# Kernel tuning notes

Hardware: AMD Instinct MI355X
Metric: run time of the kernel (lower is better)

## Reference

```python
import jax, jax.numpy as jnp
import numpy as np

D_MODEL = 1024
D_HEAD = 64
M_BITS = 32


def setup_inputs() -> dict:
    key = jax.random.key(0)
    ks = jax.random.split(key, 6)
    B, N, M = 2, 2048, 2048
    Q = jax.random.normal(ks[0], (B, N, D_MODEL), dtype=jnp.float32)
    K = jax.random.normal(ks[1], (B, M, D_MODEL), dtype=jnp.float32)
    V = jax.random.normal(ks[2], (B, M, D_MODEL), dtype=jnp.float32)
    s = 1.0 / np.sqrt(D_MODEL)
    Wq = jax.random.normal(ks[3], (D_MODEL, M_BITS), dtype=jnp.float32) * s
    Wk = jax.random.normal(ks[4], (D_MODEL, M_BITS), dtype=jnp.float32) * s
    Wv = jax.random.normal(ks[5], (D_MODEL, D_HEAD), dtype=jnp.float32) * s
    temperature = jnp.ones((1,), dtype=jnp.float32)
    return {"Q": Q, "K": K, "V": V, "Wq": Wq, "Wk": Wk, "Wv": Wv,
            "temperature": temperature}


def tropical_matmul(A, Bt):
    # A: [B, N, m], Bt: [B, M, m] (already transposed form of [B, m, M])
    # (A \odot B)_{ij} = min_k (A_ik + B_kj)
    return jnp.min(A[:, :, None, :] + Bt[:, None, :, :], axis=-1)  # [B, N, M]


def reference(Q, K, V, Wq, Wk, Wv, temperature):
    # REWA tropical encoders (continuous): linear projections to m_bits
    Qt = jnp.einsum('bnd,dm->bnm', Q, Wq)   # [B, N, m_bits]
    Kt = jnp.einsum('bsd,dm->bsm', K, Wk)   # [B, M, m_bits]
    Vp = jnp.einsum('bsd,dh->bsh', V, Wv)   # [B, M, d_head]
    # tropical (min-plus) scores, negated so shorter paths score higher
    scores = -tropical_matmul(Qt, Kt)       # [B, N, M]
    scores = scores / jax.nn.softplus(temperature[0])
    attn = jax.nn.softmax(scores, axis=-1)  # [B, N, M]
    out = jnp.einsum('bnm,bmh->bnh', attn, Vp)  # [B, N, d_head]
    return out, attn
```

## Files before the change

kernel.cpp:

```cpp
#include <hip/hip_runtime.h>
#include <math.h>

#define DM 1024
#define NB 2048
#define MBITS 32
#define DH 64

typedef __attribute__((ext_vector_type(4))) float floatx4;
typedef __attribute__((ext_vector_type(8))) short shortx8;

__device__ __forceinline__ unsigned short f32_to_bf16(float f) {
    union { float f; unsigned u; } v; v.f = f;
    unsigned r = v.u + 0x7FFF + ((v.u >> 16) & 1);
    return (unsigned short)(r >> 16);
}

__device__ __forceinline__ void split2(float x0, float x1, unsigned& hp, unsigned& lp) {
    union { float f; unsigned u; } a, b; a.f = x0; b.f = x1;
    unsigned h0 = a.u & 0xFFFF0000u, h1 = b.u & 0xFFFF0000u;
    union { unsigned u; float f; } hf0, hf1; hf0.u = h0; hf1.u = h1;
    union { float f; unsigned u; } c, d;
    c.f = x0 - hf0.f;
    d.f = x1 - hf1.f;
    hp = (h0 >> 16) | h1;
    lp = (c.u >> 16) | (d.u & 0xFFFF0000u);
}

__global__ __launch_bounds__(256) void wprep_kernel(
    const float* __restrict__ Wq, const float* __restrict__ Wk,
    const float* __restrict__ Wv, unsigned short* __restrict__ Wf)
{
    int wv = blockIdx.x * 4 + (threadIdx.x >> 6);
    int l  = threadIdx.x & 63;
    const float* W; int C, kc32, ct;
    if (wv < 64)       { W = Wq; C = 32; kc32 = wv >> 1;  ct = wv & 1; }
    else if (wv < 128) { W = Wk; C = 32; int z = wv - 64;  kc32 = z >> 1; ct = z & 1; }
    else               { W = Wv; C = 64; int z = wv - 128; kc32 = z >> 2; ct = z & 3; }
    int k0 = kc32 * 32 + (l >> 4) * 8;
    int c  = ct * 16 + (l & 15);
    float x[8];
    #pragma unroll
    for (int j = 0; j < 8; ++j) x[j] = W[(size_t)(k0 + j) * C + c];
    unsigned hp[4], lp[4];
    #pragma unroll
    for (int j2 = 0; j2 < 4; ++j2) split2(x[2 * j2], x[2 * j2 + 1], hp[j2], lp[j2]);
    uint4 hv; hv.x = hp[0]; hv.y = hp[1]; hv.z = hp[2]; hv.w = hp[3];
    uint4 lv; lv.x = lp[0]; lv.y = lp[1]; lv.z = lp[2]; lv.w = lp[3];
    *(uint4*)&Wf[(size_t)wv * 1024 + l * 8]       = hv;
    *(uint4*)&Wf[(size_t)wv * 1024 + 512 + l * 8] = lv;
}

__global__ __launch_bounds__(256) void proj_mfma2_kernel(
    const float* __restrict__ Q, const float* __restrict__ K, const float* __restrict__ V,
    const unsigned short* __restrict__ Wf,
    float* __restrict__ Qt, float* __restrict__ Kt, unsigned short* __restrict__ VpT)
{
    __shared__ float red[4][64][16];

    int gb = blockIdx.x;
    int job = gb >> 8, tile = gb & 255;
    int r0 = tile * 16;
    const float* X = (job == 0) ? Q : (job == 1) ? K : V;
    int ntct  = (job == 2) ? 4 : 2;
    int pbase = job << 6;
    int t = threadIdx.x, w = t >> 6, l = t & 63;
    int lrow = l & 15, lq = l >> 4;

    const float* xrow = &X[(size_t)(r0 + lrow) * DM + w * 256 + lq * 8];

    floatx4 acc[4];
    #pragma unroll
    for (int i = 0; i < 4; ++i) acc[i] = (floatx4){0.f, 0.f, 0.f, 0.f};

    #pragma unroll
    for (int s = 0; s < 8; ++s) {
        floatx4 g0 = *(const floatx4*)(xrow + s * 32);
        floatx4 g1 = *(const floatx4*)(xrow + s * 32 + 4);
        union { unsigned u[4]; shortx8 v; } ahi, alo;
        split2(g0.x, g0.y, ahi.u[0], alo.u[0]);
        split2(g0.z, g0.w, ahi.u[1], alo.u[1]);
        split2(g1.x, g1.y, ahi.u[2], alo.u[2]);
        split2(g1.z, g1.w, ahi.u[3], alo.u[3]);
        int kc32 = w * 8 + s;
        #pragma unroll
        for (int ct = 0; ct < 4; ++ct) {
            if (ct >= ntct) break;
            int p = pbase + kc32 * ntct + ct;
            const unsigned short* wp = &Wf[(size_t)p * 1024 + l * 8];
            shortx8 bhi = *(const shortx8*)wp;
            shortx8 blo = *(const shortx8*)(wp + 512);
            acc[ct] = __builtin_amdgcn_mfma_f32_16x16x32_bf16(ahi.v, bhi, acc[ct], 0, 0, 0);
            acc[ct] = __builtin_amdgcn_mfma_f32_16x16x32_bf16(ahi.v, blo, acc[ct], 0, 0, 0);
            acc[ct] = __builtin_amdgcn_mfma_f32_16x16x32_bf16(alo.v, bhi, acc[ct], 0, 0, 0);
        }
    }

    #pragma unroll
    for (int ct = 0; ct < 4; ++ct) {
        if (ct >= ntct) break;
        #pragma unroll
        for (int r = 0; r < 4; ++r) red[w][l][ct * 4 + r] = acc[ct][r];
    }
    __syncthreads();

    int row = r0 + lq * 4 + w;
    if (job < 2) {
        float* Y = (job == 0) ? Qt : Kt;
        #pragma unroll
        for (int ct = 0; ct < 2; ++ct) {
            float v = red[0][l][ct * 4 + w] + red[1][l][ct * 4 + w]
                    + red[2][l][ct * 4 + w] + red[3][l][ct * 4 + w];
            Y[(size_t)row * MBITS + ct * 16 + lrow] = v;
        }
    } else {
        int b = row >> 11, j = row & 2047;
        #pragma unroll
        for (int ct = 0; ct < 4; ++ct) {
            float v = red[0][l][ct * 4 + w] + red[1][l][ct * 4 + w]
                    + red[2][l][ct * 4 + w] + red[3][l][ct * 4 + w];
            VpT[(size_t)b * (DH * NB) + (size_t)(ct * 16 + lrow) * NB + j] = f32_to_bf16(v);
        }
    }
}

template <typename ET>
__global__ __launch_bounds__(256) void trop_score_kernel(
    const float* __restrict__ Qt, const float* __restrict__ Kt,
    const float* __restrict__ temp, float* __restrict__ partial,
    ET* __restrict__ ebuf)
{
    __shared__ float Qs[16][36];
    __shared__ float Ks[256][36];

    int b  = blockIdx.z;
    int jc = blockIdx.y;
    int i0 = blockIdx.x * 16;
    int t  = threadIdx.x;
    int w  = t >> 6, l = t & 63;

    if (t < 128) {
        int row = t >> 3, k4 = t & 7;
        *(floatx4*)&Qs[row][k4 * 4] =
            *(const floatx4*)&Qt[(size_t)(b * NB + i0 + row) * MBITS + k4 * 4];
    }
    #pragma unroll
    for (int u = 0; u < 8; ++u) {
        int flat4 = u * 256 + t;
        int row = flat4 >> 3, k4 = flat4 & 7;
        *(floatx4*)&Ks[row][k4 * 4] =
            *(const floatx4*)&Kt[(size_t)(b * NB + jc * 256 + row) * MBITS + k4 * 4];
    }
    float tv = temp[0];
    float c2 = -(1.0f / log1pf(__expf(tv))) * 1.44269504088896340736f;
    __syncthreads();

    float m[4][4];
    #pragma unroll
    for (int ii = 0; ii < 4; ++ii)
        #pragma unroll
        for (int jj = 0; jj < 4; ++jj) m[ii][jj] = 1e30f;

    #pragma unroll
    for (int k4 = 0; k4 < 8; ++k4) {
        floatx4 q[4], kk[4];
        #pragma unroll
        for (int ii = 0; ii < 4; ++ii) q[ii] = *(const floatx4*)&Qs[w + 4 * ii][k4 * 4];
        #pragma unroll
        for (int jj = 0; jj < 4; ++jj) kk[jj] = *(const floatx4*)&Ks[l + 64 * jj][k4 * 4];
        #pragma unroll
        for (int ii = 0; ii < 4; ++ii)
            #pragma unroll
            for (int jj = 0; jj < 4; ++jj) {
                float a0 = q[ii].x + kk[jj].x;
                float a1 = q[ii].y + kk[jj].y;
                float a2 = q[ii].z + kk[jj].z;
                float a3 = q[ii].w + kk[jj].w;
                m[ii][jj] = fminf(fminf(m[ii][jj], fminf(a0, a1)), fminf(a2, a3));
            }
    }

    float psum[4];
    #pragma unroll
    for (int ii = 0; ii < 4; ++ii) {
        int i = w + 4 * ii;
        float s = 0.f;
        #pragma unroll
        for (int jj = 0; jj < 4; ++jj) {
            int j = l + 64 * jj;
            float e = exp2f(c2 * m[ii][jj]);
            size_t idx = (size_t)(b * NB + i0 + i) * 2048 + jc * 256 + j;
            if (sizeof(ET) == 2) ebuf[idx] = (ET)f32_to_bf16(e);
            else                 ebuf[idx] = (ET)e;
            s += e;
        }
        psum[ii] = s;
    }

    #pragma unroll
    for (int ii = 0; ii < 4; ++ii) {
        float v = psum[ii];
        #pragma unroll
        for (int off = 1; off < 64; off <<= 1) v += __shfl_xor(v, off, 64);
        if (l == 0) partial[((size_t)b * NB + i0 + w + 4 * ii) * 8 + jc] = v;
    }
}

template <bool EBF16>
__global__ __launch_bounds__(256) void trop_out_kernel(
    const unsigned short* __restrict__ VpT, const float* __restrict__ partial,
    const void* __restrict__ ebuf_in, float* __restrict__ outp, float* __restrict__ attn)
{
    __shared__ unsigned short Vs[64][256];
    __shared__ unsigned short Es[16][264];
    __shared__ float inv_s[16];

    int b  = blockIdx.z;
    int jc = blockIdx.y;
    int i0 = blockIdx.x * 16;
    int t  = threadIdx.x;
    int w  = t >> 6, l = t & 63;

    #pragma unroll
    for (int u = 0; u < 8; ++u) {
        int flat16 = u * 256 + t;
        int h = flat16 >> 5, c = flat16 & 31;
        uint4 g = *(const uint4*)&VpT[(size_t)b * (DH * NB) + (size_t)h * NB + jc * 256 + c * 8];
        *(uint4*)&Vs[h][(c ^ (h & 31)) * 8] = g;
    }
    if (t < 16) {
        float s = 0.f;
        #pragma unroll
        for (int p = 0; p < 8; ++p) s += partial[((size_t)b * NB + i0 + t) * 8 + p];
        inv_s[t] = 1.0f / s;
    }

    if (EBF16) {
        const unsigned short* eb = (const unsigned short*)ebuf_in;
        #pragma unroll
        for (int u = 0; u < 2; ++u) {
            int flat = u * 256 + t;
            int row = flat >> 5, c = flat & 31;
            uint4 g = *(const uint4*)&eb[(size_t)(b * NB + i0 + row) * 2048 + jc * 256 + c * 8];
            *(uint4*)&Es[row][c * 8] = g;
        }
        __syncthreads();
        int row = t >> 4, cb = (t & 15) * 16;
        float iv = inv_s[row];
        #pragma unroll
        for (int h8 = 0; h8 < 2; ++h8) {
            uint4 e8 = *(const uint4*)&Es[row][cb + h8 * 8];
            unsigned uu[4] = {e8.x, e8.y, e8.z, e8.w};
            float f[8];
            #pragma unroll
            for (int z = 0; z < 4; ++z) {
                union { unsigned u; float f; } v0, v1;
                v0.u = uu[z] << 16; v1.u = uu[z] & 0xFFFF0000u;
                f[2 * z] = v0.f * iv; f[2 * z + 1] = v1.f * iv;
            }
            size_t gidx = (size_t)(b * NB + i0 + row) * 2048 + jc * 256 + cb + h8 * 8;
            floatx4 o0; o0.x = f[0]; o0.y = f[1]; o0.z = f[2]; o0.w = f[3];
            floatx4 o1; o1.x = f[4]; o1.y = f[5]; o1.z = f[6]; o1.w = f[7];
            *(floatx4*)&attn[gidx]     = o0;
            *(floatx4*)&attn[gidx + 4] = o1;
        }
    } else {
        __syncthreads();
        #pragma unroll
        for (int u = 0; u < 4; ++u) {
            int flat4 = u * 256 + t;
            int row = flat4 >> 6, c4 = flat4 & 63;
            size_t g = (size_t)(b * NB + i0 + row) * 2048 + jc * 256 + c4 * 4;
            floatx4 e4 = *(const floatx4*)&attn[g];
            float iv = inv_s[row];
            unsigned u0 = (unsigned)f32_to_bf16(e4.x) | ((unsigned)f32_to_bf16(e4.y) << 16);
            unsigned u1 = (unsigned)f32_to_bf16(e4.z) | ((unsigned)f32_to_bf16(e4.w) << 16);
            uint2 pk; pk.x = u0; pk.y = u1;
            *(uint2*)&Es[row][c4 * 4] = pk;
            e4.x *= iv; e4.y *= iv; e4.z *= iv; e4.w *= iv;
            *(floatx4*)&attn[g] = e4;
        }
    }
    __syncthreads();

    floatx4 acc = {0.f, 0.f, 0.f, 0.f};
    #pragma unroll
    for (int kk = 0; kk < 8; ++kk) {
        int mrow = l & 15, q4 = l >> 4;
        shortx8 a = *(const shortx8*)&Es[mrow][kk * 32 + q4 * 8];
        int h = w * 16 + mrow;
        int c = kk * 4 + q4;
        shortx8 bf = *(const shortx8*)&Vs[h][(c ^ (h & 31)) * 8];
        acc = __builtin_amdgcn_mfma_f32_16x16x32_bf16(a, bf, acc, 0, 0, 0);
    }

    #pragma unroll
    for (int r = 0; r < 4; ++r) {
        int irow = (l >> 4) * 4 + r;
        atomicAdd(&outp[(size_t)(b * NB + i0 + irow) * DH + w * 16 + (l & 15)],
                  acc[r] * inv_s[irow]);
    }
}

extern "C" void kernel_launch(void* const* d_in, const int* in_sizes, int n_in,
                              void* d_out, int out_size, void* d_ws, size_t ws_size,
                              hipStream_t stream) {
    (void)in_sizes; (void)n_in; (void)out_size;
    const float* Q    = (const float*)d_in[0];
    const float* K    = (const float*)d_in[1];
    const float* V    = (const float*)d_in[2];
    const float* Wq   = (const float*)d_in[3];
    const float* Wk   = (const float*)d_in[4];
    const float* Wv   = (const float*)d_in[5];
    const float* temp = (const float*)d_in[6];

    float* outp = (float*)d_out;
    float* attn = outp + 2 * 2048 * 64;

    char* ws = (char*)d_ws;
    float*          Qt      = (float*)(ws);
    float*          Kt      = (float*)(ws + 524288);
    float*          partial = (float*)(ws + 1048576);
    unsigned short* Wf      = (unsigned short*)(ws + 1179648);
    unsigned short* VpT     = (unsigned short*)(ws + 1703936);
    unsigned short* Ebuf    = (unsigned short*)(ws + 2228224);
    bool bf16path = ws_size >= (size_t)2228224 + 16777216;

    hipMemsetAsync(d_out, 0, 262144 * sizeof(float), stream);

    wprep_kernel<<<64, 256, 0, stream>>>(Wq, Wk, Wv, Wf);
    proj_mfma2_kernel<<<768, 256, 0, stream>>>(Q, K, V, Wf, Qt, Kt, VpT);

    if (bf16path) {
        trop_score_kernel<unsigned short><<<dim3(128, 8, 2), 256, 0, stream>>>(
            Qt, Kt, temp, partial, Ebuf);
        trop_out_kernel<true><<<dim3(128, 8, 2), 256, 0, stream>>>(
            VpT, partial, Ebuf, outp, attn);
    } else {
        trop_score_kernel<float><<<dim3(128, 8, 2), 256, 0, stream>>>(
            Qt, Kt, temp, partial, attn);
        trop_out_kernel<false><<<dim3(128, 8, 2), 256, 0, stream>>>(
            VpT, partial, attn, outp, attn);
    }
}
```

Baseline: 151.4 us.

## Fuse tropical score and attention-output kernels into one full-row block kernel

Replaces the separate score kernel (which wrote bf16 exp values and per-chunk partial sums to global memory) and the output kernel with a single 1024-thread kernel. Each block computes a full 16x2048 score row in LDS, so it can reduce row sums locally, normalise, write attn and run the PV MFMA with double-buffered V tiles. This removes the intermediate E buffer round trip, the partial-sum buffer, the memset and the atomicAdds on the output. In exchange the grid shrinks to 256 large blocks with heavy LDS use, which lowers occupancy, and Q/K are now read directly from global memory instead of staged through LDS.

After: 344.5 us. +127.6%, slower.

```diff
diff --git a/kernel.cpp b/kernel.cpp
--- a/kernel.cpp
+++ b/kernel.cpp
@@ -123,188 +123,149 @@
     }
 }
 
-template <typename ET>
-__global__ __launch_bounds__(256) void trop_score_kernel(
+__global__ __launch_bounds__(1024) void fused_score_out_kernel(
     const float* __restrict__ Qt, const float* __restrict__ Kt,
-    const float* __restrict__ temp, float* __restrict__ partial,
-    ET* __restrict__ ebuf)
+    const unsigned short* __restrict__ VpT, const float* __restrict__ temp,
+    float* __restrict__ outp, float* __restrict__ attn)
 {
-    __shared__ float Qs[16][36];
-    __shared__ float Ks[256][36];
-
-    int b  = blockIdx.z;
-    int jc = blockIdx.y;
-    int i0 = blockIdx.x * 16;
-    int t  = threadIdx.x;
-    int w  = t >> 6, l = t & 63;
-
-    if (t < 128) {
-        int row = t >> 3, k4 = t & 7;
-        *(floatx4*)&Qs[row][k4 * 4] =
-            *(const floatx4*)&Qt[(size_t)(b * NB + i0 + row) * MBITS + k4 * 4];
-    }
-    #pragma unroll
-    for (int u = 0; u < 8; ++u) {
-        int flat4 = u * 256 + t;
-        int row = flat4 >> 3, k4 = flat4 & 7;
-        *(floatx4*)&Ks[row][k4 * 4] =
-            *(const floatx4*)&Kt[(size_t)(b * NB + jc * 256 + row) * MBITS + k4 * 4];
-    }
-    float tv = temp[0];
-    float c2 = -(1.0f / log1pf(__expf(tv))) * 1.44269504088896340736f;
-    __syncthreads();
-
-    float m[4][4];
-    #pragma unroll
-    for (int ii = 0; ii < 4; ++ii)
-        #pragma unroll
-        for (int jj = 0; jj < 4; ++jj) m[ii][jj] = 1e30f;
+    __shared__ unsigned short Elds[16][2056];
+    __shared__ unsigned short Vsb[2][64][256];
+    __shared__ float redsum[16][8];
+    __shared__ float inv_s[16];
+    __shared__ float redC[16][64][4];
+
+    const int b  = blockIdx.y;
+    const int i0 = blockIdx.x * 16;
+    const int t  = threadIdx.x;
+    const int w  = t >> 6, l = t & 63;
+    const int wr = w & 1;
+    const int wj = w >> 1;
+    const int jb = wj * 256 + l * 4;
+
+    const float tv = temp[0];
+    const float c2 = -(1.0f / log1pf(__expf(tv))) * 1.44269504088896340736f;
+
+    const float* Krow = &Kt[(size_t)(b * NB + jb) * MBITS];
+    const float* Qrow = &Qt[(size_t)(b * NB + i0 + wr * 8) * MBITS];
+
+    float m[8][4];
+    #pragma unroll
+    for (int r = 0; r < 8; ++r)
+        #pragma unroll
+        for (int jj = 0; jj < 4; ++jj) m[r][jj] = 1e30f;
 
     #pragma unroll
     for (int k4 = 0; k4 < 8; ++k4) {
-        floatx4 q[4], kk[4];
-        #pragma unroll
-        for (int ii = 0; ii < 4; ++ii) q[ii] = *(const floatx4*)&Qs[w + 4 * ii][k4 * 4];
-        #pragma unroll
-        for (int jj = 0; jj < 4; ++jj) kk[jj] = *(const floatx4*)&Ks[l + 64 * jj][k4 * 4];
-        #pragma unroll
-        for (int ii = 0; ii < 4; ++ii)
+        floatx4 kk[4];
+        #pragma unroll
+        for (int jj = 0; jj < 4; ++jj)
+            kk[jj] = *(const floatx4*)&Krow[jj * MBITS + k4 * 4];
+        #pragma unroll
+        for (int r = 0; r < 8; ++r) {
+            floatx4 q = *(const floatx4*)&Qrow[r * MBITS + k4 * 4];
             #pragma unroll
             for (int jj = 0; jj < 4; ++jj) {
-                float a0 = q[ii].x + kk[jj].x;
-                float a1 = q[ii].y + kk[jj].y;
-                float a2 = q[ii].z + kk[jj].z;
-                float a3 = q[ii].w + kk[jj].w;
-                m[ii][jj] = fminf(fminf(m[ii][jj], fminf(a0, a1)), fminf(a2, a3));
+                float a0 = q.x + kk[jj].x;
+                float a1 = q.y + kk[jj].y;
+                float a2 = q.z + kk[jj].z;
+                float a3 = q.w + kk[jj].w;
+                m[r][jj] = fminf(fminf(m[r][jj], fminf(a0, a1)), fminf(a2, a3));
             }
-    }
-
-    float psum[4];
-    #pragma unroll
-    for (int ii = 0; ii < 4; ++ii) {
-        int i = w + 4 * ii;
-        float s = 0.f;
-        #pragma unroll
-        for (int jj = 0; jj < 4; ++jj) {
-            int j = l + 64 * jj;
-            float e = exp2f(c2 * m[ii][jj]);
-            size_t idx = (size_t)(b * NB + i0 + i) * 2048 + jc * 256 + j;
-            if (sizeof(ET) == 2) ebuf[idx] = (ET)f32_to_bf16(e);
-            else                 ebuf[idx] = (ET)e;
-            s += e;
-        }
-        psum[ii] = s;
-    }
-
-    #pragma unroll
-    for (int ii = 0; ii < 4; ++ii) {
-        float v = psum[ii];
-        #pragma unroll
-        for (int off = 1; off < 64; off <<= 1) v += __shfl_xor(v, off, 64);
-        if (l == 0) partial[((size_t)b * NB + i0 + w + 4 * ii) * 8 + jc] = v;
-    }
-}
-
-template <bool EBF16>
-__global__ __launch_bounds__(256) void trop_out_kernel(
-    const unsigned short* __restrict__ VpT, const float* __restrict__ partial,
-    const void* __restrict__ ebuf_in, float* __restrict__ outp, float* __restrict__ attn)
-{
-    __shared__ unsigned short Vs[64][256];
-    __shared__ unsigned short Es[16][264];
-    __shared__ float inv_s[16];
-
-    int b  = blockIdx.z;
-    int jc = blockIdx.y;
-    int i0 = blockIdx.x * 16;
-    int t  = threadIdx.x;
-    int w  = t >> 6, l = t & 63;
-
-    #pragma unroll
-    for (int u = 0; u < 8; ++u) {
-        int flat16 = u * 256 + t;
-        int h = flat16 >> 5, c = flat16 & 31;
-        uint4 g = *(const uint4*)&VpT[(size_t)b * (DH * NB) + (size_t)h * NB + jc * 256 + c * 8];
-        *(uint4*)&Vs[h][(c ^ (h & 31)) * 8] = g;
-    }
+        }
+    }
+
+    #pragma unroll
+    for (int r = 0; r < 8; ++r) {
+        float e0 = exp2f(c2 * m[r][0]);
+        float e1 = exp2f(c2 * m[r][1]);
+        float e2 = exp2f(c2 * m[r][2]);
+        float e3 = exp2f(c2 * m[r][3]);
+        uint2 pk;
+        pk.x = (unsigned)f32_to_bf16(e0) | ((unsigned)f32_to_bf16(e1) << 16);
+        pk.y = (unsigned)f32_to_bf16(e2) | ((unsigned)f32_to_bf16(e3) << 16);
+        *(uint2*)&Elds[wr * 8 + r][jb] = pk;
+        float s = (e0 + e1) + (e2 + e3);
+        #pragma unroll
+        for (int off = 1; off < 64; off <<= 1) s += __shfl_xor(s, off, 64);
+        if (l == 0) redsum[w][r] = s;
+    }
+    __syncthreads();
+
     if (t < 16) {
         float s = 0.f;
         #pragma unroll
-        for (int p = 0; p < 8; ++p) s += partial[((size_t)b * NB + i0 + t) * 8 + p];
+        for (int g = 0; g < 8; ++g) s += redsum[(t >> 3) + 2 * g][t & 7];
         inv_s[t] = 1.0f / s;
     }
 
-    if (EBF16) {
-        const unsigned short* eb = (const unsigned short*)ebuf_in;
-        #pragma unroll
-        for (int u = 0; u < 2; ++u) {
-            int flat = u * 256 + t;
-            int row = flat >> 5, c = flat & 31;
-            uint4 g = *(const uint4*)&eb[(size_t)(b * NB + i0 + row) * 2048 + jc * 256 + c * 8];
-            *(uint4*)&Es[row][c * 8] = g;
+    const int sh = t >> 5, sc = t & 31;
+    {
+        uint4 g0 = *(const uint4*)&VpT[(size_t)b * (DH * NB) + (size_t)sh * NB + sc * 8];
+        uint4 g1 = *(const uint4*)&VpT[(size_t)b * (DH * NB) + (size_t)(sh + 32) * NB + sc * 8];
+        *(uint4*)&Vsb[0][sh][(sc ^ (sh & 31)) * 8]             = g0;
+        *(uint4*)&Vsb[0][sh + 32][(sc ^ ((sh + 32) & 31)) * 8] = g1;
+    }
+    __syncthreads();
+
+    const int mrow = l & 15, q4 = l >> 4;
+    const int hh  = (w & 3) * 16 + mrow;
+    const int kg  = w >> 2;
+    const int vsw = hh & 31;
+    const float iv = inv_s[w];
+    floatx4 acc = {0.f, 0.f, 0.f, 0.f};
+    int pb = 0;
+
+    for (int jc2 = 0; jc2 < 8; ++jc2) {
+        uint4 g0, g1;
+        if (jc2 < 7) {
+            g0 = *(const uint4*)&VpT[(size_t)b * (DH * NB) + (size_t)sh * NB + (jc2 + 1) * 256 + sc * 8];
+            g1 = *(const uint4*)&VpT[(size_t)b * (DH * NB) + (size_t)(sh + 32) * NB + (jc2 + 1) * 256 + sc * 8];
+        }
+        #pragma unroll
+        for (int t2 = 0; t2 < 2; ++t2) {
+            int ks = kg * 2 + t2;
+            shortx8 a = *(const shortx8*)&Elds[mrow][jc2 * 256 + ks * 32 + q4 * 8];
+            int c = ks * 4 + q4;
+            shortx8 bf = *(const shortx8*)&Vsb[pb][hh][(c ^ vsw) * 8];
+            acc = __builtin_amdgcn_mfma_f32_16x16x32_bf16(a, bf, acc, 0, 0, 0);
+        }
+        {
+            uint2 pk = *(const uint2*)&Elds[w][jc2 * 256 + l * 4];
+            union { unsigned u; float f; } x0, x1, x2, x3;
+            x0.u = pk.x << 16; x1.u = pk.x & 0xFFFF0000u;
+            x2.u = pk.y << 16; x3.u = pk.y & 0xFFFF0000u;
+            floatx4 o;
+            o.x = x0.f * iv; o.y = x1.f * iv; o.z = x2.f * iv; o.w = x3.f * iv;
+            *(floatx4*)&attn[(size_t)(b * NB + i0 + w) * 2048 + jc2 * 256 + l * 4] = o;
+        }
+        if (jc2 < 7) {
+            *(uint4*)&Vsb[pb ^ 1][sh][(sc ^ (sh & 31)) * 8]             = g0;
+            *(uint4*)&Vsb[pb ^ 1][sh + 32][(sc ^ ((sh + 32) & 31)) * 8] = g1;
         }
         __syncthreads();
-        int row = t >> 4, cb = (t & 15) * 16;
-        float iv = inv_s[row];
-        #pragma unroll
-        for (int h8 = 0; h8 < 2; ++h8) {
-            uint4 e8 = *(const uint4*)&Es[row][cb + h8 * 8];
-            unsigned uu[4] = {e8.x, e8.y, e8.z, e8.w};
-            float f[8];
-            #pragma unroll
-            for (int z = 0; z < 4; ++z) {
-                union { unsigned u; float f; } v0, v1;
-                v0.u = uu[z] << 16; v1.u = uu[z] & 0xFFFF0000u;
-                f[2 * z] = v0.f * iv; f[2 * z + 1] = v1.f * iv;
-            }
-            size_t gidx = (size_t)(b * NB + i0 + row) * 2048 + jc * 256 + cb + h8 * 8;
-            floatx4 o0; o0.x = f[0]; o0.y = f[1]; o0.z = f[2]; o0.w = f[3];
-            floatx4 o1; o1.x = f[4]; o1.y = f[5]; o1.z = f[6]; o1.w = f[7];
-            *(floatx4*)&attn[gidx]     = o0;
-            *(floatx4*)&attn[gidx + 4] = o1;
-        }
-    } else {
-        __syncthreads();
-        #pragma unroll
-        for (int u = 0; u < 4; ++u) {
-            int flat4 = u * 256 + t;
-            int row = flat4 >> 6, c4 = flat4 & 63;
-            size_t g = (size_t)(b * NB + i0 + row) * 2048 + jc * 256 + c4 * 4;
-            floatx4 e4 = *(const floatx4*)&attn[g];
-            float iv = inv_s[row];
-            unsigned u0 = (unsigned)f32_to_bf16(e4.x) | ((unsigned)f32_to_bf16(e4.y) << 16);
-            unsigned u1 = (unsigned)f32_to_bf16(e4.z) | ((unsigned)f32_to_bf16(e4.w) << 16);
-            uint2 pk; pk.x = u0; pk.y = u1;
-            *(uint2*)&Es[row][c4 * 4] = pk;
-            e4.x *= iv; e4.y *= iv; e4.z *= iv; e4.w *= iv;
-            *(floatx4*)&attn[g] = e4;
-        }
-    }
-    __syncthreads();
-
-    floatx4 acc = {0.f, 0.f, 0.f, 0.f};
-    #pragma unroll
-    for (int kk = 0; kk < 8; ++kk) {
-        int mrow = l & 15, q4 = l >> 4;
-        shortx8 a = *(const shortx8*)&Es[mrow][kk * 32 + q4 * 8];
-        int h = w * 16 + mrow;
-        int c = kk * 4 + q4;
-        shortx8 bf = *(const shortx8*)&Vs[h][(c ^ (h & 31)) * 8];
-        acc = __builtin_amdgcn_mfma_f32_16x16x32_bf16(a, bf, acc, 0, 0, 0);
-    }
-
-    #pragma unroll
-    for (int r = 0; r < 4; ++r) {
-        int irow = (l >> 4) * 4 + r;
-        atomicAdd(&outp[(size_t)(b * NB + i0 + irow) * DH + w * 16 + (l & 15)],
-                  acc[r] * inv_s[irow]);
+        pb ^= 1;
+    }
+
+    *(floatx4*)&redC[w][l][0] = acc;
+    __syncthreads();
+    if (w < 4) {
+        floatx4 v0 = *(const floatx4*)&redC[w][l][0];
+        floatx4 v1 = *(const floatx4*)&redC[w + 4][l][0];
+        floatx4 v2 = *(const floatx4*)&redC[w + 8][l][0];
+        floatx4 v3 = *(const floatx4*)&redC[w + 12][l][0];
+        #pragma unroll
+        for (int r = 0; r < 4; ++r) {
+            int irow = q4 * 4 + r;
+            float v = (v0[r] + v1[r]) + (v2[r] + v3[r]);
+            outp[(size_t)(b * NB + i0 + irow) * DH + w * 16 + mrow] = v * inv_s[irow];
+        }
     }
 }
 
 extern "C" void kernel_launch(void* const* d_in, const int* in_sizes, int n_in,
                               void* d_out, int out_size, void* d_ws, size_t ws_size,
                               hipStream_t stream) {
-    (void)in_sizes; (void)n_in; (void)out_size;
+    (void)in_sizes; (void)n_in; (void)out_size; (void)ws_size;
     const float* Q    = (const float*)d_in[0];
     const float* K    = (const float*)d_in[1];
     const float* V    = (const float*)d_in[2];
@@ -317,28 +278,12 @@
     float* attn = outp + 2 * 2048 * 64;
 
     char* ws = (char*)d_ws;
-    float*          Qt      = (float*)(ws);
-    float*          Kt      = (float*)(ws + 524288);
-    float*          partial = (float*)(ws + 1048576);
-    unsigned short* Wf      = (unsigned short*)(ws + 1179648);
-    unsigned short* VpT     = (unsigned short*)(ws + 1703936);
-    unsigned short* Ebuf    = (unsigned short*)(ws + 2228224);
-    bool bf16path = ws_size >= (size_t)2228224 + 16777216;
-
-    hipMemsetAsync(d_out, 0, 262144 * sizeof(float), stream);
+    float*          Qt  = (float*)(ws);
+    float*          Kt  = (float*)(ws + 524288);
+    unsigned short* Wf  = (unsigned short*)(ws + 1179648);
+    unsigned short* VpT = (unsigned short*)(ws + 1703936);
 
     wprep_kernel<<<64, 256, 0, stream>>>(Wq, Wk, Wv, Wf);
     proj_mfma2_kernel<<<768, 256, 0, stream>>>(Q, K, V, Wf, Qt, Kt, VpT);
-
-    if (bf16path) {
-        trop_score_kernel<unsigned short><<<dim3(128, 8, 2), 256, 0, stream>>>(
-            Qt, Kt, temp, partial, Ebuf);
-        trop_out_kernel<true><<<dim3(128, 8, 2), 256, 0, stream>>>(
-            VpT, partial, Ebuf, outp, attn);
-    } else {
-        trop_score_kernel<float><<<dim3(128, 8, 2), 256, 0, stream>>>(
-            Qt, Kt, temp, partial, attn);
-        trop_out_kernel<false><<<dim3(128, 8, 2), 256, 0, stream>>>(
-            VpT, partial, attn, outp, attn);
-    }
-}
+    fused_score_out_kernel<<<dim3(128, 2), 1024, 0, stream>>>(Qt, Kt, VpT, temp, outp, attn);
+}
```
